# Optimization experiments

Hardware: AMD Instinct MI355X
Metric: run time of the kernel (lower is better)

## Reference

```python
import jax, jax.numpy as jnp
import numpy as np

B = 512      # batch
H = 64       # latent_dim == GRU hidden size
F = 32       # n_features
S = 2048     # seq_len
NEG_SLOPE = 0.01  # nn.LeakyReLU default


def setup_inputs() -> dict:
    key = jax.random.key(0)
    ks = jax.random.split(key, 14)

    def p(k, shape, scale=0.1):
        return jax.random.normal(k, shape, dtype=jnp.float32) * scale

    return {
        "noise": jax.random.normal(ks[0], (B, H), dtype=jnp.float32),
        # GRU forward direction (layer 0): weight_ih_l0, weight_hh_l0, biases
        "W_ih_f": p(ks[1], (3 * H, H)),
        "W_hh_f": p(ks[2], (3 * H, H)),
        "b_ih_f": p(ks[3], (3 * H,)),
        "b_hh_f": p(ks[4], (3 * H,)),
        # GRU backward direction (layer 0 reverse)
        "W_ih_b": p(ks[5], (3 * H, H)),
        "W_hh_b": p(ks[6], (3 * H, H)),
        "b_ih_b": p(ks[7], (3 * H,)),
        "b_hh_b": p(ks[8], (3 * H,)),
        # latent_linear: Linear(2H -> H)
        "W_lat": p(ks[9], (H, 2 * H)),
        "b_lat": p(ks[10], (H,)),
        # output_linear: Linear(H -> F)
        "W_out": p(ks[11], (F, H)),
        "b_out": p(ks[12], (F,)),
    }


def _leaky(x):
    return jnp.where(x >= 0, x, NEG_SLOPE * x)


def _gru_cell(x, h, W_ih, W_hh, b_ih, b_hh):
    # PyTorch GRU cell: gates ordered (r, z, n)
    gi = x @ W_ih.T + b_ih          # (B, 3H)
    gh = h @ W_hh.T + b_hh          # (B, 3H)
    i_r, i_z, i_n = jnp.split(gi, 3, axis=-1)
    h_r, h_z, h_n = jnp.split(gh, 3, axis=-1)
    r = jax.nn.sigmoid(i_r + h_r)
    z = jax.nn.sigmoid(i_z + h_z)
    n = jnp.tanh(i_n + r * h_n)
    return (1.0 - z) * n + z * h


def reference(noise, W_ih_f, W_hh_f, b_ih_f, b_hh_f,
              W_ih_b, W_hh_b, b_ih_b, b_hh_b,
              W_lat, b_lat, W_out, b_out):
    # hidden_state = noise.repeat((D*n_layers,1,1)) -> both directions start at noise
    batch = noise.shape[0]

    def step(carry, _):
        x, hf, hb = carry
        # GRU on a length-1 sequence: each direction does one cell update;
        # output timestep = concat(fwd_out, bwd_out)
        hf2 = _gru_cell(x, hf, W_ih_f, W_hh_f, b_ih_f, b_hh_f)
        hb2 = _gru_cell(x, hb, W_ih_b, W_hh_b, b_ih_b, b_hh_b)
        out = jnp.concatenate([hf2, hb2], axis=-1)        # (B, 2H)
        lat = _leaky(out @ W_lat.T + b_lat)               # (B, H)
        return (lat, hf2, hb2), lat

    x0 = jnp.zeros((batch, H), dtype=noise.dtype)
    _, ys = jax.lax.scan(step, (x0, noise, noise), None, length=S)
    seq = jnp.transpose(ys, (1, 0, 2))   # (B, S, H)
    seq = _leaky(seq)                    # second LeakyReLU as in the original
    out = jax.nn.sigmoid(seq @ W_out.T + b_out)  # (B, S, F)
    return out
```

## Files before the change

### kernel.cpp

```cpp
#include <hip/hip_runtime.h>
#include <hip/hip_bf16.h>


#define NBATCH 512
#define NH 64
#define NS 2048
#define NF 32
#define MROW 16
#define LDH 72

typedef short s16x8 __attribute__((ext_vector_type(8)));
typedef float f32x4 __attribute__((ext_vector_type(4)));

#define MFMA(a, b, c) __builtin_amdgcn_mfma_f32_16x16x32_bf16((a), (b), (c), 0, 0, 0)

#define NLOG2E  (-1.4426950408889634f)
#define N2LOG2E (-2.8853900817779268f)

__device__ __forceinline__ short f2bf(float f) {
    return (short)((__float_as_uint(f) + 0x8000u) >> 16);
}

__device__ __forceinline__ f32x4 v_exp2(f32x4 a) {
    f32x4 r;
#pragma unroll
    for (int i = 0; i < 4; ++i) r[i] = __builtin_amdgcn_exp2f(a[i]);
    return r;
}

__device__ __forceinline__ f32x4 v_rcp(f32x4 a) {
    f32x4 r;
#pragma unroll
    for (int i = 0; i < 4; ++i) r[i] = __builtin_amdgcn_rcpf(a[i]);
    return r;
}

__device__ __forceinline__ f32x4 v_lk(f32x4 a) {
    f32x4 b = a * 0.01f;
    f32x4 r;
#pragma unroll
    for (int i = 0; i < 4; ++i) r[i] = fmaxf(a[i], b[i]);
    return r;
}

__device__ __forceinline__ f32x4 v_sigm(f32x4 a) {
    return v_rcp(v_exp2(a * NLOG2E) + 1.0f);
}

__device__ __forceinline__ int2 pk4bf(f32x4 v) {
    union { __hip_bfloat162 b; int i; } lo, hi;
    float2 a; a.x = v[0]; a.y = v[1];
    float2 b; b.x = v[2]; b.y = v[3];
    lo.b = __float22bfloat162_rn(a);
    hi.b = __float22bfloat162_rn(b);
    int2 r; r.x = lo.i; r.y = hi.i;
    return r;
}

__device__ __forceinline__ s16x8 bfragW(const float* __restrict__ W, int ldk,
                                        int row, int kf, int quad) {
    const float* p = W + (size_t)row * ldk + kf * 32 + quad * 8;
    s16x8 r;
#pragma unroll
    for (int i = 0; i < 8; ++i) r[i] = f2bf(p[i]);
    return r;
}

__device__ __forceinline__ f32x4 bias4(const float* __restrict__ p) {
    const float4 v = *(const float4*)p;
    f32x4 r = {v.x, v.y, v.z, v.w};
    return r;
}

__global__ __launch_bounds__(1024)
void grugan_kernel(const float* __restrict__ noise,
                   const float* __restrict__ Wihf, const float* __restrict__ Whhf,
                   const float* __restrict__ bihf, const float* __restrict__ bhhf,
                   const float* __restrict__ Wihb, const float* __restrict__ Whhb,
                   const float* __restrict__ bihb, const float* __restrict__ bhhb,
                   const float* __restrict__ Wlat, const float* __restrict__ blat,
                   const float* __restrict__ Wout, const float* __restrict__ bout,
                   float* __restrict__ out)
{
    __shared__ __align__(16) short Xs[2][MROW][LDH];
    __shared__ __align__(16) short X2s[2][MROW][LDH];
    __shared__ __align__(16) short Hs[2][2][MROW][LDH];

    const int tid  = threadIdx.x;
    const int wave = tid >> 6;
    const int lane = tid & 63;
    const int n    = lane & 15;
    const int quad = lane >> 4;
    const int row0 = blockIdx.x * MROW;

    for (int idx = tid; idx < MROW * LDH; idx += 1024) (&Xs[0][0][0])[idx] = 0;
    f32x4 hreg = {0.f, 0.f, 0.f, 0.f};
    const int gdir = wave >> 2;
    const int gjq  = (wave & 3) * 16 + quad * 4;
    if (wave < 8) {
        const float4 nz = *(const float4*)&noise[(size_t)(row0 + n) * NH + gjq];
        hreg[0] = nz.x; hreg[1] = nz.y; hreg[2] = nz.z; hreg[3] = nz.w;
        *(int2*)&Hs[0][gdir][n][gjq] = pk4bf(hreg);
    }
    __syncthreads();

    if (wave < 8) {
        const int dir  = gdir;
        const int cb   = wave & 3;
        const int jrow = cb * 16 + n;
        const int jq   = gjq;
        const float* Wih = dir ? Wihb : Wihf;
        const float* Whh = dir ? Whhb : Whhf;
        const float* bih = dir ? bihb : bihf;
        const float* bhh = dir ? bhhb : bhhf;

        s16x8 wir0 = bfragW(Wih, NH,   0 + jrow, 0, quad);
        s16x8 wir1 = bfragW(Wih, NH,   0 + jrow, 1, quad);
        s16x8 wiz0 = bfragW(Wih, NH,  64 + jrow, 0, quad);
        s16x8 wiz1 = bfragW(Wih, NH,  64 + jrow, 1, quad);
        s16x8 win0 = bfragW(Wih, NH, 128 + jrow, 0, quad);
        s16x8 win1 = bfragW(Wih, NH, 128 + jrow, 1, quad);
        s16x8 whr0 = bfragW(Whh, NH,   0 + jrow, 0, quad);
        s16x8 whr1 = bfragW(Whh, NH,   0 + jrow, 1, quad);
        s16x8 whz0 = bfragW(Whh, NH,  64 + jrow, 0, quad);
        s16x8 whz1 = bfragW(Whh, NH,  64 + jrow, 1, quad);
        s16x8 whn0 = bfragW(Whh, NH, 128 + jrow, 0, quad);
        s16x8 whn1 = bfragW(Whh, NH, 128 + jrow, 1, quad);
        f32x4 initR, initZ;
        {
            f32x4 a = bias4(&bih[jq]),      b = bias4(&bhh[jq]);
            initR = a + b;
            f32x4 c = bias4(&bih[64 + jq]), d = bias4(&bhh[64 + jq]);
            initZ = c + d;
        }
        const f32x4 initN1 = bias4(&bih[128 + jq]);
        const f32x4 initN2 = bias4(&bhh[128 + jq]);

        f32x4 accR, accZ, accN2;
        {
            s16x8 ha0 = *(const s16x8*)&Hs[0][dir][n][quad * 8];
            s16x8 ha1 = *(const s16x8*)&Hs[0][dir][n][32 + quad * 8];
            accR  = MFMA(whr0, ha0, initR);  accR  = MFMA(whr1, ha1, accR);
            accZ  = MFMA(whz0, ha0, initZ);  accZ  = MFMA(whz1, ha1, accZ);
            accN2 = MFMA(whn0, ha0, initN2); accN2 = MFMA(whn1, ha1, accN2);
        }

#define GSTEP(HB) do {                                                          \
        s16x8 xa0 = *(const s16x8*)&Xs[HB][n][quad * 8];                        \
        s16x8 xa1 = *(const s16x8*)&Xs[HB][n][32 + quad * 8];                   \
        accR = MFMA(wir0, xa0, accR);   accR = MFMA(wir1, xa1, accR);           \
        accZ = MFMA(wiz0, xa0, accZ);   accZ = MFMA(wiz1, xa1, accZ);           \
        f32x4 accN1 = MFMA(win0, xa0, initN1);                                  \
        accN1 = MFMA(win1, xa1, accN1);                                         \
        f32x4 eR = v_exp2(accR * NLOG2E);                                       \
        f32x4 rr = v_rcp(eR + 1.0f);                                            \
        f32x4 u  = accN1 + rr * accN2;                                          \
        f32x4 eU = v_exp2(u * N2LOG2E);                                         \
        f32x4 eZ = v_exp2(accZ * NLOG2E);                                       \
        f32x4 numer = (eZ + hreg) + eU * (hreg - eZ);                           \
        f32x4 denom = (eU + 1.0f) * (eZ + 1.0f);                                \
        hreg = numer * v_rcp(denom);                                            \
        *(int2*)&Hs[(HB) ^ 1][dir][n][jq] = pk4bf(hreg);                        \
        __syncthreads();                                \
        {                                                                       \
            s16x8 ha0 = *(const s16x8*)&Hs[(HB) ^ 1][dir][n][quad * 8];         \
            s16x8 ha1 = *(const s16x8*)&Hs[(HB) ^ 1][dir][n][32 + quad * 8];    \
            accR  = MFMA(whr0, ha0, initR);  accR  = MFMA(whr1, ha1, accR);     \
            accZ  = MFMA(whz0, ha0, initZ);  accZ  = MFMA(whz1, ha1, accZ);     \
            accN2 = MFMA(whn0, ha0, initN2); accN2 = MFMA(whn1, ha1, accN2);    \
        }                                                                       \
        __syncthreads();                                \
    } while (0)

        for (int t = 0; t < NS; t += 2) {
            GSTEP(0);
            GSTEP(1);
        }
#undef GSTEP
    } else if (wave < 12) {
        const int lt = wave & 3;
        const int nq = lt * 16 + quad * 4;
        s16x8 wl0 = bfragW(Wlat, 2 * NH, lt * 16 + n, 0, quad);
        s16x8 wl1 = bfragW(Wlat, 2 * NH, lt * 16 + n, 1, quad);
        s16x8 wl2 = bfragW(Wlat, 2 * NH, lt * 16 + n, 2, quad);
        s16x8 wl3 = bfragW(Wlat, 2 * NH, lt * 16 + n, 3, quad);
        const f32x4 initL = bias4(&blat[lt * 16 + quad * 4]);

#define LSTEP(HB) do {                                                          \
        __syncthreads();                                \
        s16x8 fa0 = *(const s16x8*)&Hs[(HB) ^ 1][0][n][quad * 8];               \
        s16x8 fa1 = *(const s16x8*)&Hs[(HB) ^ 1][0][n][32 + quad * 8];          \
        s16x8 ba0 = *(const s16x8*)&Hs[(HB) ^ 1][1][n][quad * 8];               \
        s16x8 ba1 = *(const s16x8*)&Hs[(HB) ^ 1][1][n][32 + quad * 8];          \
        f32x4 lac = MFMA(wl0, fa0, initL);                                      \
        lac = MFMA(wl1, fa1, lac);                                              \
        lac = MFMA(wl2, ba0, lac);                                              \
        lac = MFMA(wl3, ba1, lac);                                              \
        f32x4 la = v_lk(lac);                                                   \
        *(int2*)&Xs[(HB) ^ 1][n][nq]  = pk4bf(la);                              \
        *(int2*)&X2s[(HB) ^ 1][n][nq] = pk4bf(v_lk(la));                        \
        __syncthreads();                                \
    } while (0)

        for (int t = 0; t < NS; t += 2) {
            LSTEP(0);
            LSTEP(1);
        }
#undef LSTEP
    } else if (wave < 14) {
        const int f0 = (wave & 1) * 16;
        s16x8 wo0 = bfragW(Wout, NH, f0 + n, 0, quad);
        s16x8 wo1 = bfragW(Wout, NH, f0 + n, 1, quad);
        const f32x4 initO = bias4(&bout[f0 + quad * 4]);
        float* const orow = out + (size_t)(row0 + n) * (NS * NF) + f0 + quad * 4;
        f32x4 yv = {0.f, 0.f, 0.f, 0.f};

#define OSTEP(HB, T) do {                                                       \
        if ((T) >= 2)                                                           \
            *(f32x4*)(orow + (size_t)((T) - 2) * NF) = yv;                      \
        __syncthreads();                                                \
        if ((T) >= 1) {                                                         \
            s16x8 p0 = *(const s16x8*)&X2s[HB][n][quad * 8];                    \
            s16x8 p1 = *(const s16x8*)&X2s[HB][n][32 + quad * 8];               \
            f32x4 po = MFMA(wo0, p0, initO);                                    \
            po = MFMA(wo1, p1, po);                                             \
            yv = v_sigm(po);                                                    \
        }                                                                       \
        __syncthreads();                                                \
    } while (0)

        for (int t = 0; t < NS; t += 2) {
            OSTEP(0, t);
            OSTEP(1, t + 1);
        }
#undef OSTEP

        *(f32x4*)(orow + (size_t)(NS - 2) * NF) = yv;
        s16x8 p0 = *(const s16x8*)&X2s[0][n][quad * 8];
        s16x8 p1 = *(const s16x8*)&X2s[0][n][32 + quad * 8];
        f32x4 po = MFMA(wo0, p0, initO);
        po = MFMA(wo1, p1, po);
        *(f32x4*)(orow + (size_t)(NS - 1) * NF) = v_sigm(po);
    } else {
#pragma unroll 1
        for (int i = 0; i < 2 * NS; ++i) __syncthreads();
    }
}

extern "C" void kernel_launch(void* const* d_in, const int* in_sizes, int n_in,
                              void* d_out, int out_size, void* d_ws, size_t ws_size,
                              hipStream_t stream) {
    const float* noise = (const float*)d_in[0];
    const float* Wihf  = (const float*)d_in[1];
    const float* Whhf  = (const float*)d_in[2];
    const float* bihf  = (const float*)d_in[3];
    const float* bhhf  = (const float*)d_in[4];
    const float* Wihb  = (const float*)d_in[5];
    const float* Whhb  = (const float*)d_in[6];
    const float* bihb  = (const float*)d_in[7];
    const float* bhhb  = (const float*)d_in[8];
    const float* Wlat  = (const float*)d_in[9];
    const float* blat  = (const float*)d_in[10];
    const float* Wout  = (const float*)d_in[11];
    const float* bout  = (const float*)d_in[12];

    grugan_kernel<<<dim3(NBATCH / MROW), dim3(1024), 0, stream>>>(
        noise, Wihf, Whhf, bihf, bhhf, Wihb, Whhb, bihb, bhhb,
        Wlat, blat, Wout, bout, (float*)d_out);
}
```

Baseline: 1.613 ms.

## Replace __syncthreads with LDS-only barriers and restructure output and latent steps

Swaps __syncthreads for a custom barrier that waits only on LDS counters (lgkmcnt), so pending global stores no longer stall every barrier. The output waves now store each sigmoid result right away instead of deferring it one step. The latent matmul is split into two independent MFMA chains to shorten the dependency chain. Weights are pinned in registers with empty asm and waves_per_eu is set. The risk is subtle ordering issues if any barrier actually depended on global memory, plus changed register allocation.

```diff
diff --git a/kernel.cpp b/kernel.cpp
--- a/kernel.cpp
+++ b/kernel.cpp
@@ -16,6 +16,12 @@
 
 #define NLOG2E  (-1.4426950408889634f)
 #define N2LOG2E (-2.8853900817779268f)
+
+#define PIN(x) __asm__("" : "+v"(x))
+
+__device__ __forceinline__ void bar_lds() {
+    __asm__ volatile("s_waitcnt lgkmcnt(0)\n\ts_barrier" ::: "memory");
+}
 
 __device__ __forceinline__ short f2bf(float f) {
     return (short)((__float_as_uint(f) + 0x8000u) >> 16);
@@ -73,6 +79,7 @@
 }
 
 __global__ __launch_bounds__(1024)
+__attribute__((amdgpu_waves_per_eu(4, 4)))
 void grugan_kernel(const float* __restrict__ noise,
                    const float* __restrict__ Wihf, const float* __restrict__ Whhf,
                    const float* __restrict__ bihf, const float* __restrict__ bhhf,
@@ -133,8 +140,11 @@
             f32x4 c = bias4(&bih[64 + jq]), d = bias4(&bhh[64 + jq]);
             initZ = c + d;
         }
-        const f32x4 initN1 = bias4(&bih[128 + jq]);
-        const f32x4 initN2 = bias4(&bhh[128 + jq]);
+        f32x4 initN1 = bias4(&bih[128 + jq]);
+        f32x4 initN2 = bias4(&bhh[128 + jq]);
+        PIN(wir0); PIN(wir1); PIN(wiz0); PIN(wiz1); PIN(win0); PIN(win1);
+        PIN(whr0); PIN(whr1); PIN(whz0); PIN(whz1); PIN(whn0); PIN(whn1);
+        PIN(initR); PIN(initZ); PIN(initN1); PIN(initN2);
 
         f32x4 accR, accZ, accN2;
         {
@@ -161,7 +171,7 @@
         f32x4 denom = (eU + 1.0f) * (eZ + 1.0f);                                \
         hreg = numer * v_rcp(denom);                                            \
         *(int2*)&Hs[(HB) ^ 1][dir][n][jq] = pk4bf(hreg);                        \
-        __syncthreads();                                \
+        bar_lds();                                      \
         {                                                                       \
             s16x8 ha0 = *(const s16x8*)&Hs[(HB) ^ 1][dir][n][quad * 8];         \
             s16x8 ha1 = *(const s16x8*)&Hs[(HB) ^ 1][dir][n][32 + quad * 8];    \
@@ -169,7 +179,7 @@
             accZ  = MFMA(whz0, ha0, initZ);  accZ  = MFMA(whz1, ha1, accZ);     \
             accN2 = MFMA(whn0, ha0, initN2); accN2 = MFMA(whn1, ha1, accN2);    \
         }                                                                       \
-        __syncthreads();                                \
+        bar_lds();                                      \
     } while (0)
 
         for (int t = 0; t < NS; t += 2) {
@@ -184,22 +194,24 @@
         s16x8 wl1 = bfragW(Wlat, 2 * NH, lt * 16 + n, 1, quad);
         s16x8 wl2 = bfragW(Wlat, 2 * NH, lt * 16 + n, 2, quad);
         s16x8 wl3 = bfragW(Wlat, 2 * NH, lt * 16 + n, 3, quad);
-        const f32x4 initL = bias4(&blat[lt * 16 + quad * 4]);
+        f32x4 initL = bias4(&blat[lt * 16 + quad * 4]);
+        PIN(wl0); PIN(wl1); PIN(wl2); PIN(wl3); PIN(initL);
+        const f32x4 Z4 = {0.f, 0.f, 0.f, 0.f};
 
 #define LSTEP(HB) do {                                                          \
-        __syncthreads();                                \
+        bar_lds();                                      \
         s16x8 fa0 = *(const s16x8*)&Hs[(HB) ^ 1][0][n][quad * 8];               \
         s16x8 fa1 = *(const s16x8*)&Hs[(HB) ^ 1][0][n][32 + quad * 8];          \
         s16x8 ba0 = *(const s16x8*)&Hs[(HB) ^ 1][1][n][quad * 8];               \
         s16x8 ba1 = *(const s16x8*)&Hs[(HB) ^ 1][1][n][32 + quad * 8];          \
-        f32x4 lac = MFMA(wl0, fa0, initL);                                      \
-        lac = MFMA(wl1, fa1, lac);                                              \
-        lac = MFMA(wl2, ba0, lac);                                              \
-        lac = MFMA(wl3, ba1, lac);                                              \
-        f32x4 la = v_lk(lac);                                                   \
+        f32x4 c1 = MFMA(wl0, fa0, initL);                                       \
+        c1 = MFMA(wl1, fa1, c1);                                                \
+        f32x4 c2 = MFMA(wl2, ba0, Z4);                                          \
+        c2 = MFMA(wl3, ba1, c2);                                                \
+        f32x4 la = v_lk(c1 + c2);                                               \
         *(int2*)&Xs[(HB) ^ 1][n][nq]  = pk4bf(la);                              \
         *(int2*)&X2s[(HB) ^ 1][n][nq] = pk4bf(v_lk(la));                        \
-        __syncthreads();                                \
+        bar_lds();                                      \
     } while (0)
 
         for (int t = 0; t < NS; t += 2) {
@@ -211,22 +223,20 @@
         const int f0 = (wave & 1) * 16;
         s16x8 wo0 = bfragW(Wout, NH, f0 + n, 0, quad);
         s16x8 wo1 = bfragW(Wout, NH, f0 + n, 1, quad);
-        const f32x4 initO = bias4(&bout[f0 + quad * 4]);
+        f32x4 initO = bias4(&bout[f0 + quad * 4]);
+        PIN(wo0); PIN(wo1); PIN(initO);
         float* const orow = out + (size_t)(row0 + n) * (NS * NF) + f0 + quad * 4;
-        f32x4 yv = {0.f, 0.f, 0.f, 0.f};
 
 #define OSTEP(HB, T) do {                                                       \
-        if ((T) >= 2)                                                           \
-            *(f32x4*)(orow + (size_t)((T) - 2) * NF) = yv;                      \
-        __syncthreads();                                                \
         if ((T) >= 1) {                                                         \
             s16x8 p0 = *(const s16x8*)&X2s[HB][n][quad * 8];                    \
             s16x8 p1 = *(const s16x8*)&X2s[HB][n][32 + quad * 8];               \
             f32x4 po = MFMA(wo0, p0, initO);                                    \
             po = MFMA(wo1, p1, po);                                             \
-            yv = v_sigm(po);                                                    \
+            *(f32x4*)(orow + (size_t)((T) - 1) * NF) = v_sigm(po);              \
         }                                                                       \
-        __syncthreads();                                                \
+        bar_lds();                                                      \
+        bar_lds();                                                      \
     } while (0)
 
         for (int t = 0; t < NS; t += 2) {
@@ -235,7 +245,6 @@
         }
 #undef OSTEP
 
-        *(f32x4*)(orow + (size_t)(NS - 2) * NF) = yv;
         s16x8 p0 = *(const s16x8*)&X2s[0][n][quad * 8];
         s16x8 p1 = *(const s16x8*)&X2s[0][n][32 + quad * 8];
         f32x4 po = MFMA(wo0, p0, initO);
@@ -243,7 +252,7 @@
         *(f32x4*)(orow + (size_t)(NS - 1) * NF) = v_sigm(po);
     } else {
 #pragma unroll 1
-        for (int i = 0; i < 2 * NS; ++i) __syncthreads();
+        for (int i = 0; i < 2 * NS; ++i) bar_lds();
     }
 }
 
```

Result: no change. 1.621 ms (+0.5%).
